# Performance work log

Hardware: AMD Instinct MI355X
Metric: run time of the kernel (lower is better)

## Reference

```python
import jax, jax.numpy as jnp
import numpy as np

NUM_HEADS = 12
HEAD_SIZE = 64  # hidden_size // num_heads


def setup_inputs() -> dict:
    key = jax.random.key(0)
    ks = jax.random.split(key, 4)
    B, S, H = 2, 2048, 768
    return {
        "hidden_states": jax.random.normal(ks[0], (B, S, H), dtype=jnp.float32),
        "attention_mask": jnp.ones((B, S), dtype=jnp.int32),
        "Wq": jax.random.normal(ks[1], (H, H), dtype=jnp.float32) * 0.02,
        "bq": jnp.zeros((H,), dtype=jnp.float32),
        "Wk": jax.random.normal(ks[2], (H, H), dtype=jnp.float32) * 0.02,
        "bk": jnp.zeros((H,), dtype=jnp.float32),
        "Wv": jax.random.normal(ks[3], (H, H), dtype=jnp.float32) * 0.02,
        "bv": jnp.zeros((H,), dtype=jnp.float32),
    }


def reference(hidden_states, attention_mask, Wq, bq, Wk, bk, Wv, bv):
    B, S, H = hidden_states.shape
    nh, hs = NUM_HEADS, HEAD_SIZE

    def to_heads(x):  # [B,S,H] -> [nh,B,S,hs] (matches to_multi_head)
        return x.reshape(B, S, nh, hs).transpose(2, 0, 1, 3)

    # torch Linear: y = x @ W.T + b
    q = to_heads(hidden_states @ Wq.T + bq)
    k = to_heads(hidden_states @ Wk.T + bk)
    v = to_heads(hidden_states @ Wv.T + bv)

    scores = jnp.einsum("hbqd,hbkd->hbqk", q, k) / jnp.float32(hs) ** 0.5
    # mask: 1 -> attend, 0 -> -inf; broadcast over query dim
    m = 1.0 - attention_mask.astype(scores.dtype)
    add = jnp.where(m != 0.0, -jnp.inf, 0.0)[None, :, None, :]  # [1,B,1,S]
    probs = jax.nn.softmax(scores + add, axis=-1)
    # dropout is identity in eval mode
    out = jnp.einsum("hbqk,hbkd->hbqd", probs, v)
    # from_multi_head: [nh,B,S,hs] -> [B,S,H]
    return out.transpose(1, 2, 0, 3).reshape(B, S, H)
```

## Files before the change

### kernel.cpp

```cpp
#include <hip/hip_runtime.h>
#include <hip/hip_bf16.h>

#define BATCH 2
#define SEQ   2048
#define HID   768
#define NH    12
#define HS    64
#define MROWS (BATCH*SEQ)
#define N3    (3*HID)
#define HB    (NH*BATCH)

typedef __attribute__((ext_vector_type(8))) short short8;
typedef __attribute__((ext_vector_type(4))) float floatx4;

#define QSCALE 0.1803368801111204f

__device__ __forceinline__ unsigned short f2bf(float x){
  __hip_bfloat16 h = __float2bfloat16(x);
  return __builtin_bit_cast(unsigned short, h);
}
__device__ __forceinline__ void glds16(const unsigned short* g, unsigned short* l){
  __builtin_amdgcn_global_load_lds(
    (const __attribute__((address_space(1))) unsigned int*)g,
    (__attribute__((address_space(3))) unsigned int*)l, 16, 0, 0);
}

__global__ void f2bf_all_kernel(const float* __restrict__ X,
                                const float* __restrict__ Wq,
                                const float* __restrict__ Wk,
                                const float* __restrict__ Wv,
                                unsigned short* __restrict__ Xb,
                                unsigned short* __restrict__ Wb){
  const int XQ = MROWS*HID/4;
  const int WQ = HID*HID/4;
  int i = blockIdx.x * 256 + threadIdx.x;
  const float* src; unsigned short* dst; int off;
  if(i < XQ){ src = X; dst = Xb; off = i; }
  else {
    int j = i - XQ;
    int w = j / WQ; off = j - w*WQ;
    src = (w==0) ? Wq : (w==1) ? Wk : Wv;
    dst = Wb + (size_t)w*HID*HID;
  }
  float4 v = reinterpret_cast<const float4*>(src)[off];
  ushort4 o;
  o.x = f2bf(v.x); o.y = f2bf(v.y); o.z = f2bf(v.z); o.w = f2bf(v.w);
  reinterpret_cast<ushort4*>(dst)[off] = o;
}

__global__ __launch_bounds__(256) void qkv_gemm_kernel(
    const unsigned short* __restrict__ Xb,
    const unsigned short* __restrict__ Wb,
    const float* __restrict__ bq, const float* __restrict__ bk, const float* __restrict__ bv,
    unsigned short* __restrict__ Qb, unsigned short* __restrict__ Kb,
    unsigned short* __restrict__ Vtb)
{
  __shared__ __align__(16) union {
    struct { unsigned short A[2][128][32]; unsigned short B[2][128][32]; } s;
    unsigned short T[4][64][72];
  } u;
  const int m0 = blockIdx.y << 7;
  const int n0 = blockIdx.x << 7;
  const int tid  = threadIdx.x;
  const int wave = tid >> 6, lane = tid & 63;
  const int wr = wave >> 1, wc = wave & 1;
  const int quad = lane >> 4, l15 = lane & 15;

  const unsigned short* gsrc[4];
  unsigned short* ldst[4];
  #pragma unroll
  for(int p=0;p<4;p++){
    int ck  = ((p&1)<<8) + tid;
    int row = ck>>2, c = ck&3, pc = c ^ (row&3);
    if(p<2){ gsrc[p] = Xb + (size_t)(m0+row)*HID + (pc<<3); ldst[p] = &u.s.A[0][row][c<<3]; }
    else   { gsrc[p] = Wb + (size_t)(n0+row)*HID + (pc<<3); ldst[p] = &u.s.B[0][row][c<<3]; }
  }

  floatx4 acc[4][4];
  #pragma unroll
  for(int i=0;i<4;i++)
    #pragma unroll
    for(int j=0;j<4;j++) acc[i][j] = (floatx4){0.f,0.f,0.f,0.f};

  auto stage = [&](int buf, int k0){
    const int bo = buf*(128*32);
    #pragma unroll
    for(int p=0;p<4;p++) glds16(gsrc[p] + k0, ldst[p] + bo);
  };

  stage(0, 0);
  __syncthreads();

  const int swa = l15 & 3;
  for(int t=0;t<HID/32;t++){
    const int buf = t & 1;
    if(t < HID/32 - 1) stage(buf^1, (t+1)*32);
    short8 a[4], b[4];
    #pragma unroll
    for(int i=0;i<4;i++)
      a[i] = *reinterpret_cast<const short8*>(&u.s.A[buf][wr*64+i*16+l15][(quad^swa)<<3]);
    #pragma unroll
    for(int j=0;j<4;j++)
      b[j] = *reinterpret_cast<const short8*>(&u.s.B[buf][wc*64+j*16+l15][(quad^swa)<<3]);
    #pragma unroll
    for(int i=0;i<4;i++)
      #pragma unroll
      for(int j=0;j<4;j++)
        acc[i][j] = __builtin_amdgcn_mfma_f32_16x16x32_bf16(a[i], b[j], acc[i][j], 0, 0, 0);
    __syncthreads();
  }

  const int which = n0 / HID;
  if(which < 2){
    unsigned short* dst = which==0 ? Qb : Kb;
    const float* bias = which==0 ? bq : bk;
    const float scale = which==0 ? QSCALE : 1.0f;
    #pragma unroll
    for(int j=0;j<4;j++){
      const int nn = n0 - which*HID + wc*64 + j*16 + l15;
      const int head = nn >> 6, d = nn & 63;
      const float bb = bias[nn];
      #pragma unroll
      for(int i=0;i<4;i++){
        #pragma unroll
        for(int r=0;r<4;r++){
          const int m = m0 + wr*64 + i*16 + quad*4 + r;
          const int b_ = m >> 11, s = m & 2047;
          const int hb = head*BATCH + b_;
          dst[((size_t)(hb<<11) + s)*HS + d] = f2bf((acc[i][j][r] + bb)*scale);
        }
      }
    }
  } else {
    const int nbase = n0 - 2*HID + wc*64;
    const int head = nbase >> 6;
    const int b_ = m0 >> 11;
    const int hbv = head*BATCH + b_;
    const int s0 = (m0 & 2047) + wr*64;
    #pragma unroll
    for(int j=0;j<4;j++){
      const float bb = bv[nbase + j*16 + l15];
      #pragma unroll
      for(int i=0;i<4;i++){
        unsigned int lo = (unsigned int)f2bf(acc[i][j][0]+bb) | ((unsigned int)f2bf(acc[i][j][1]+bb)<<16);
        unsigned int hi = (unsigned int)f2bf(acc[i][j][2]+bb) | ((unsigned int)f2bf(acc[i][j][3]+bb)<<16);
        uint2 pk; pk.x = lo; pk.y = hi;
        *reinterpret_cast<uint2*>(&u.T[wave][j*16+l15][i*16 + quad*4]) = pk;
      }
    }
    #pragma unroll
    for(int p=0;p<8;p++){
      const int d = p*8 + (lane>>3), cm = lane & 7;
      uint4 v = *reinterpret_cast<const uint4*>(&u.T[wave][d][cm*8]);
      *reinterpret_cast<uint4*>(Vtb + ((size_t)(hbv*HS) + d)*SEQ + s0 + cm*8) = v;
    }
  }
}

__global__ __launch_bounds__(256) void attn_kernel(
    const unsigned short* __restrict__ Qb,
    const unsigned short* __restrict__ Kb,
    const unsigned short* __restrict__ Vtb,
    const int* __restrict__ mask,
    float* __restrict__ out)
{
  __shared__ __align__(16) unsigned short Ks2 [2][64][64];
  __shared__ __align__(16) unsigned short Vts2[2][64][64];
  __shared__ __align__(16) unsigned short Ps  [4][16][72];
  __shared__ float maskadd[SEQ];

  const int bid = blockIdx.x;
  const int hb = bid >> 5, qt = bid & 31, q0 = qt << 6;
  const int tid = threadIdx.x, wave = tid >> 6, lane = tid & 63;
  const int quad = lane >> 4, l15 = lane & 15;
  const int b_ = hb & 1, head = hb >> 1;

  const unsigned short* gK[2]; const unsigned short* gV[2];
  unsigned short* lK[2]; unsigned short* lV[2];
  #pragma unroll
  for(int p=0;p<2;p++){
    int ck = (p<<8) + tid;
    int row = ck>>3, c = ck&7, pc = c ^ (row&7);
    gK[p] = Kb  + ((size_t)(hb<<11) + row)*HS + (pc<<3);
    lK[p] = &Ks2[0][row][c<<3];
    gV[p] = Vtb + ((size_t)(hb*HS) + row)*SEQ + (pc<<3);
    lV[p] = &Vts2[0][row][c<<3];
  }
  auto stage = [&](int buf, int k0){
    const int bo = buf*(64*64);
    #pragma unroll
    for(int p=0;p<2;p++){
      glds16(gK[p] + (size_t)k0*HS, lK[p] + bo);
      glds16(gV[p] + k0,           lV[p] + bo);
    }
  };

  stage(0, 0);

  for(int i=tid;i<SEQ;i+=256)
    maskadd[i] = mask[(b_<<11) + i] ? 0.f : -1e30f;

  short8 a_q[2];
  {
    const unsigned short* qsrc = Qb + ((size_t)(hb<<11) + q0 + wave*16 + l15)*HS;
    a_q[0] = *reinterpret_cast<const short8*>(qsrc + quad*8);
    a_q[1] = *reinterpret_cast<const short8*>(qsrc + 32 + quad*8);
  }

  float lsum[4] = {0.f, 0.f, 0.f, 0.f};
  floatx4 o_acc[4];
  #pragma unroll
  for(int dt=0;dt<4;dt++) o_acc[dt] = (floatx4){0.f,0.f,0.f,0.f};

  __syncthreads();

  const int sw = l15 & 7;
  for(int t=0;t<SEQ/64;t++){
    const int buf = t & 1, k0 = t << 6;
    if(t < SEQ/64 - 1) stage(buf^1, k0 + 64);

    const unsigned short (*Kst)[64]  = Ks2[buf];
    const unsigned short (*Vst)[64]  = Vts2[buf];

    #pragma unroll
    for(int kt=0;kt<4;kt++){
      floatx4 sacc = (floatx4){0.f,0.f,0.f,0.f};
      #pragma unroll
      for(int c=0;c<2;c++){
        short8 bk_ = *reinterpret_cast<const short8*>(
            &Kst[kt*16 + l15][(((c<<2)+quad)^sw)<<3]);
        sacc = __builtin_amdgcn_mfma_f32_16x16x32_bf16(a_q[c], bk_, sacc, 0, 0, 0);
      }
      const float ma = maskadd[k0 + kt*16 + l15];
      #pragma unroll
      for(int r=0;r<4;r++){
        float p = exp2f(sacc[r] + ma);
        lsum[r] += p;
        Ps[wave][quad*4+r][kt*16 + l15] = f2bf(p);
      }
    }

    #pragma unroll
    for(int c=0;c<2;c++){
      short8 ap = *reinterpret_cast<const short8*>(&Ps[wave][l15][c*32 + quad*8]);
      #pragma unroll
      for(int dt=0;dt<4;dt++){
        short8 bv_ = *reinterpret_cast<const short8*>(
            &Vst[dt*16 + l15][(((c<<2)+quad)^sw)<<3]);
        o_acc[dt] = __builtin_amdgcn_mfma_f32_16x16x32_bf16(ap, bv_, o_acc[dt], 0, 0, 0);
      }
    }
    __syncthreads();
  }

  #pragma unroll
  for(int x=1;x<16;x<<=1)
    #pragma unroll
    for(int r=0;r<4;r++) lsum[r] += __shfl_xor(lsum[r], x);

  float inv[4];
  #pragma unroll
  for(int r=0;r<4;r++) inv[r] = 1.0f / lsum[r];
  #pragma unroll
  for(int dt=0;dt<4;dt++){
    #pragma unroll
    for(int r=0;r<4;r++){
      const int srow = q0 + wave*16 + quad*4 + r;
      out[((size_t)(b_<<11) + srow)*HID + (head<<6) + dt*16 + l15] =
        o_acc[dt][r] * inv[r];
    }
  }
}

extern "C" void kernel_launch(void* const* d_in, const int* in_sizes, int n_in,
                              void* d_out, int out_size, void* d_ws, size_t ws_size,
                              hipStream_t stream) {
  const float* X    = (const float*)d_in[0];
  const int*   mask = (const int*)  d_in[1];
  const float* Wq   = (const float*)d_in[2];
  const float* bq   = (const float*)d_in[3];
  const float* Wk   = (const float*)d_in[4];
  const float* bk   = (const float*)d_in[5];
  const float* Wv   = (const float*)d_in[6];
  const float* bv   = (const float*)d_in[7];
  float* out = (float*)d_out;

  unsigned short* Xb  = (unsigned short*)d_ws;
  unsigned short* Wb  = Xb  + (size_t)MROWS*HID;
  unsigned short* Qb  = Wb  + (size_t)N3*HID;
  unsigned short* Kb  = Qb  + (size_t)HB*SEQ*HS;
  unsigned short* Vtb = Kb  + (size_t)HB*SEQ*HS;

  const int total_quads = (MROWS*HID + 3*HID*HID)/4;
  f2bf_all_kernel<<<total_quads/256, 256, 0, stream>>>(X, Wq, Wk, Wv, Xb, Wb);

  qkv_gemm_kernel<<<dim3(N3/128, MROWS/128), 256, 0, stream>>>(
      Xb, Wb, bq, bk, bv, Qb, Kb, Vtb);

  attn_kernel<<<HB*32, 256, 0, stream>>>(Qb, Kb, Vtb, mask, out);
}
```

Measured before the change: 180.4 us.

## Precompute mask flags, load V directly to registers, coalesce Q/K stores

An extra block in the conversion kernel precomputes the additive mask and per-64-key-tile flags, so the attention kernel skips the mask add on unmasked tiles and no longer fills a shared mask array per block. V fragments are now read straight from global memory into registers instead of being staged through LDS, which shrinks LDS use. The S-tile MFMA operand order is swapped so P can be written as packed 64-bit stores. The GEMM epilogue routes Q/K through LDS for coalesced 16-byte stores. The trade-off is uncached, unpipelined global loads of V in the inner loop, which could add latency.

Measured after the change: 213.5 us. 1.18x slower.

```diff
diff --git a/kernel.cpp b/kernel.cpp
--- a/kernel.cpp
+++ b/kernel.cpp
@@ -29,11 +29,27 @@
                                 const float* __restrict__ Wq,
                                 const float* __restrict__ Wk,
                                 const float* __restrict__ Wv,
+                                const int* __restrict__ mask,
                                 unsigned short* __restrict__ Xb,
-                                unsigned short* __restrict__ Wb){
+                                unsigned short* __restrict__ Wb,
+                                float* __restrict__ maskaddG,
+                                int* __restrict__ flagsG){
   const int XQ = MROWS*HID/4;
   const int WQ = HID*HID/4;
-  int i = blockIdx.x * 256 + threadIdx.x;
+  const int NB = (XQ + 3*WQ)/256;
+  const int tid = threadIdx.x;
+  if(blockIdx.x == NB){
+    for(int i=tid;i<BATCH*SEQ;i+=256) maskaddG[i] = mask[i] ? 0.f : -1e30f;
+    if(tid < BATCH*32){
+      int b = tid >> 5, t = tid & 31;
+      const int* mrow = mask + b*SEQ + t*64;
+      int any = 0;
+      for(int i=0;i<64;i++) any |= (mrow[i]==0);
+      flagsG[tid] = any;
+    }
+    return;
+  }
+  int i = blockIdx.x * 256 + tid;
   const float* src; unsigned short* dst; int off;
   if(i < XQ){ src = X; dst = Xb; off = i; }
   else {
@@ -111,32 +127,31 @@
   }
 
   const int which = n0 / HID;
+  const int nbase = n0 - which*HID + wc*64;
+  const int head  = nbase >> 6;
+  const int b_    = m0 >> 11;
+  const int hb    = head*BATCH + b_;
+  const int s0    = (m0 & 2047) + wr*64;
   if(which < 2){
     unsigned short* dst = which==0 ? Qb : Kb;
     const float* bias = which==0 ? bq : bk;
     const float scale = which==0 ? QSCALE : 1.0f;
     #pragma unroll
     for(int j=0;j<4;j++){
-      const int nn = n0 - which*HID + wc*64 + j*16 + l15;
-      const int head = nn >> 6, d = nn & 63;
-      const float bb = bias[nn];
-      #pragma unroll
-      for(int i=0;i<4;i++){
+      const float bb = bias[nbase + j*16 + l15];
+      #pragma unroll
+      for(int i=0;i<4;i++)
         #pragma unroll
-        for(int r=0;r<4;r++){
-          const int m = m0 + wr*64 + i*16 + quad*4 + r;
-          const int b_ = m >> 11, s = m & 2047;
-          const int hb = head*BATCH + b_;
-          dst[((size_t)(hb<<11) + s)*HS + d] = f2bf((acc[i][j][r] + bb)*scale);
-        }
-      }
+        for(int r=0;r<4;r++)
+          u.T[wave][i*16 + quad*4 + r][j*16 + l15] = f2bf((acc[i][j][r] + bb)*scale);
+    }
+    #pragma unroll
+    for(int p=0;p<8;p++){
+      const int row = p*8 + (lane>>3), dc = (lane&7)*8;
+      uint4 v = *reinterpret_cast<const uint4*>(&u.T[wave][row][dc]);
+      *reinterpret_cast<uint4*>(dst + ((size_t)(hb<<11) + s0 + row)*HS + dc) = v;
     }
   } else {
-    const int nbase = n0 - 2*HID + wc*64;
-    const int head = nbase >> 6;
-    const int b_ = m0 >> 11;
-    const int hbv = head*BATCH + b_;
-    const int s0 = (m0 & 2047) + wr*64;
     #pragma unroll
     for(int j=0;j<4;j++){
       const float bb = bv[nbase + j*16 + l15];
@@ -152,7 +167,7 @@
     for(int p=0;p<8;p++){
       const int d = p*8 + (lane>>3), cm = lane & 7;
       uint4 v = *reinterpret_cast<const uint4*>(&u.T[wave][d][cm*8]);
-      *reinterpret_cast<uint4*>(Vtb + ((size_t)(hbv*HS) + d)*SEQ + s0 + cm*8) = v;
+      *reinterpret_cast<uint4*>(Vtb + ((size_t)(hb*HS) + d)*SEQ + s0 + cm*8) = v;
     }
   }
 }
@@ -161,13 +176,12 @@
     const unsigned short* __restrict__ Qb,
     const unsigned short* __restrict__ Kb,
     const unsigned short* __restrict__ Vtb,
-    const int* __restrict__ mask,
+    const float* __restrict__ maskaddG,
+    const int* __restrict__ flagsG,
     float* __restrict__ out)
 {
-  __shared__ __align__(16) unsigned short Ks2 [2][64][64];
-  __shared__ __align__(16) unsigned short Vts2[2][64][64];
-  __shared__ __align__(16) unsigned short Ps  [4][16][72];
-  __shared__ float maskadd[SEQ];
+  __shared__ __align__(16) unsigned short Ks2[2][64][64];
+  __shared__ __align__(16) unsigned short Ps2[4][16][72];
 
   const int bid = blockIdx.x;
   const int hb = bid >> 5, qt = bid & 31, q0 = qt << 6;
@@ -175,30 +189,21 @@
   const int quad = lane >> 4, l15 = lane & 15;
   const int b_ = hb & 1, head = hb >> 1;
 
-  const unsigned short* gK[2]; const unsigned short* gV[2];
-  unsigned short* lK[2]; unsigned short* lV[2];
+  const unsigned short* gK[2]; unsigned short* lK[2];
   #pragma unroll
   for(int p=0;p<2;p++){
     int ck = (p<<8) + tid;
     int row = ck>>3, c = ck&7, pc = c ^ (row&7);
-    gK[p] = Kb  + ((size_t)(hb<<11) + row)*HS + (pc<<3);
+    gK[p] = Kb + ((size_t)(hb<<11) + row)*HS + (pc<<3);
     lK[p] = &Ks2[0][row][c<<3];
-    gV[p] = Vtb + ((size_t)(hb*HS) + row)*SEQ + (pc<<3);
-    lV[p] = &Vts2[0][row][c<<3];
-  }
-  auto stage = [&](int buf, int k0){
+  }
+  auto stageK = [&](int buf, int k0){
     const int bo = buf*(64*64);
     #pragma unroll
-    for(int p=0;p<2;p++){
-      glds16(gK[p] + (size_t)k0*HS, lK[p] + bo);
-      glds16(gV[p] + k0,           lV[p] + bo);
-    }
+    for(int p=0;p<2;p++) glds16(gK[p] + (size_t)k0*HS, lK[p] + bo);
   };
 
-  stage(0, 0);
-
-  for(int i=tid;i<SEQ;i+=256)
-    maskadd[i] = mask[(b_<<11) + i] ? 0.f : -1e30f;
+  stageK(0, 0);
 
   short8 a_q[2];
   {
@@ -207,67 +212,93 @@
     a_q[1] = *reinterpret_cast<const short8*>(qsrc + 32 + quad*8);
   }
 
-  float lsum[4] = {0.f, 0.f, 0.f, 0.f};
+  float lsum4[4] = {0.f,0.f,0.f,0.f};
   floatx4 o_acc[4];
   #pragma unroll
   for(int dt=0;dt<4;dt++) o_acc[dt] = (floatx4){0.f,0.f,0.f,0.f};
+
+  const unsigned short* vbase = Vtb + (size_t)(hb*HS)*SEQ;
 
   __syncthreads();
 
   const int sw = l15 & 7;
   for(int t=0;t<SEQ/64;t++){
     const int buf = t & 1, k0 = t << 6;
-    if(t < SEQ/64 - 1) stage(buf^1, k0 + 64);
-
-    const unsigned short (*Kst)[64]  = Ks2[buf];
-    const unsigned short (*Vst)[64]  = Vts2[buf];
-
+    if(t < SEQ/64 - 1) stageK(buf^1, k0 + 64);
+
+    short8 vf[4][2];
+    #pragma unroll
+    for(int dt=0;dt<4;dt++)
+      #pragma unroll
+      for(int c=0;c<2;c++)
+        vf[dt][c] = *reinterpret_cast<const short8*>(
+            vbase + (size_t)(dt*16 + l15)*SEQ + k0 + c*32 + quad*8);
+
+    const unsigned short (*Kst)[64] = Ks2[buf];
+
+    floatx4 st[4];
     #pragma unroll
     for(int kt=0;kt<4;kt++){
-      floatx4 sacc = (floatx4){0.f,0.f,0.f,0.f};
+      st[kt] = (floatx4){0.f,0.f,0.f,0.f};
       #pragma unroll
       for(int c=0;c<2;c++){
-        short8 bk_ = *reinterpret_cast<const short8*>(
+        short8 kf = *reinterpret_cast<const short8*>(
             &Kst[kt*16 + l15][(((c<<2)+quad)^sw)<<3]);
-        sacc = __builtin_amdgcn_mfma_f32_16x16x32_bf16(a_q[c], bk_, sacc, 0, 0, 0);
+        st[kt] = __builtin_amdgcn_mfma_f32_16x16x32_bf16(kf, a_q[c], st[kt], 0, 0, 0);
       }
-      const float ma = maskadd[k0 + kt*16 + l15];
-      #pragma unroll
-      for(int r=0;r<4;r++){
-        float p = exp2f(sacc[r] + ma);
-        lsum[r] += p;
-        Ps[wave][quad*4+r][kt*16 + l15] = f2bf(p);
+    }
+
+    const bool masked = (flagsG[(b_<<5) + t] != 0);
+    if(!masked){
+      #pragma unroll
+      for(int kt=0;kt<4;kt++){
+        float p0 = exp2f(st[kt][0]), p1 = exp2f(st[kt][1]);
+        float p2 = exp2f(st[kt][2]), p3 = exp2f(st[kt][3]);
+        lsum4[0] += p0; lsum4[1] += p1; lsum4[2] += p2; lsum4[3] += p3;
+        uint2 pk;
+        pk.x = (unsigned int)f2bf(p0) | ((unsigned int)f2bf(p1)<<16);
+        pk.y = (unsigned int)f2bf(p2) | ((unsigned int)f2bf(p3)<<16);
+        *reinterpret_cast<uint2*>(&Ps2[wave][l15][kt*16 + quad*4]) = pk;
       }
-    }
-
-    #pragma unroll
-    for(int c=0;c<2;c++){
-      short8 ap = *reinterpret_cast<const short8*>(&Ps[wave][l15][c*32 + quad*8]);
-      #pragma unroll
-      for(int dt=0;dt<4;dt++){
-        short8 bv_ = *reinterpret_cast<const short8*>(
-            &Vst[dt*16 + l15][(((c<<2)+quad)^sw)<<3]);
-        o_acc[dt] = __builtin_amdgcn_mfma_f32_16x16x32_bf16(ap, bv_, o_acc[dt], 0, 0, 0);
+    } else {
+      #pragma unroll
+      for(int kt=0;kt<4;kt++){
+        float4 ma = *reinterpret_cast<const float4*>(
+            maskaddG + (b_<<11) + k0 + kt*16 + quad*4);
+        float p0 = exp2f(st[kt][0] + ma.x), p1 = exp2f(st[kt][1] + ma.y);
+        float p2 = exp2f(st[kt][2] + ma.z), p3 = exp2f(st[kt][3] + ma.w);
+        lsum4[0] += p0; lsum4[1] += p1; lsum4[2] += p2; lsum4[3] += p3;
+        uint2 pk;
+        pk.x = (unsigned int)f2bf(p0) | ((unsigned int)f2bf(p1)<<16);
+        pk.y = (unsigned int)f2bf(p2) | ((unsigned int)f2bf(p3)<<16);
+        *reinterpret_cast<uint2*>(&Ps2[wave][l15][kt*16 + quad*4]) = pk;
       }
     }
+
+    short8 ap0 = *reinterpret_cast<const short8*>(&Ps2[wave][l15][quad*8]);
+    short8 ap1 = *reinterpret_cast<const short8*>(&Ps2[wave][l15][32 + quad*8]);
+    #pragma unroll
+    for(int dt=0;dt<4;dt++){
+      o_acc[dt] = __builtin_amdgcn_mfma_f32_16x16x32_bf16(ap0, vf[dt][0], o_acc[dt], 0, 0, 0);
+      o_acc[dt] = __builtin_amdgcn_mfma_f32_16x16x32_bf16(ap1, vf[dt][1], o_acc[dt], 0, 0, 0);
+    }
     __syncthreads();
   }
 
-  #pragma unroll
-  for(int x=1;x<16;x<<=1)
-    #pragma unroll
-    for(int r=0;r<4;r++) lsum[r] += __shfl_xor(lsum[r], x);
-
-  float inv[4];
-  #pragma unroll
-  for(int r=0;r<4;r++) inv[r] = 1.0f / lsum[r];
+  float lsum = (lsum4[0]+lsum4[1]) + (lsum4[2]+lsum4[3]);
+  lsum += __shfl_xor(lsum, 16);
+  lsum += __shfl_xor(lsum, 32);
+  float linv[4];
+  #pragma unroll
+  for(int r=0;r<4;r++) linv[r] = 1.0f / __shfl(lsum, quad*4 + r);
+
   #pragma unroll
   for(int dt=0;dt<4;dt++){
     #pragma unroll
     for(int r=0;r<4;r++){
       const int srow = q0 + wave*16 + quad*4 + r;
       out[((size_t)(b_<<11) + srow)*HID + (head<<6) + dt*16 + l15] =
-        o_acc[dt][r] * inv[r];
+        o_acc[dt][r] * linv[r];
     }
   }
 }
@@ -290,12 +321,15 @@
   unsigned short* Qb  = Wb  + (size_t)N3*HID;
   unsigned short* Kb  = Qb  + (size_t)HB*SEQ*HS;
   unsigned short* Vtb = Kb  + (size_t)HB*SEQ*HS;
+  float* maskaddG = (float*)(Vtb + (size_t)HB*SEQ*HS);
+  int*   flagsG   = (int*)(maskaddG + MROWS);
 
   const int total_quads = (MROWS*HID + 3*HID*HID)/4;
-  f2bf_all_kernel<<<total_quads/256, 256, 0, stream>>>(X, Wq, Wk, Wv, Xb, Wb);
+  f2bf_all_kernel<<<total_quads/256 + 1, 256, 0, stream>>>(
+      X, Wq, Wk, Wv, mask, Xb, Wb, maskaddG, flagsG);
 
   qkv_gemm_kernel<<<dim3(N3/128, MROWS/128), 256, 0, stream>>>(
       Xb, Wb, bq, bk, bv, Qb, Kb, Vtb);
 
-  attn_kernel<<<HB*32, 256, 0, stream>>>(Qb, Kb, Vtb, mask, out);
-}
+  attn_kernel<<<HB*32, 256, 0, stream>>>(Qb, Kb, Vtb, maskaddG, flagsG, out);
+}
```
